# Kernel optimization log

Hardware: AMD Instinct MI355X
Metric: run time of the kernel (lower is better)

The kernel has to match this reference:

```python
import jax, jax.numpy as jnp
import numpy as np

UNITS = 1024
IN_DIM = 1024
BATCH = 8192


def setup_inputs() -> dict:
    key = jax.random.key(0)
    ks = jax.random.split(key, 8)
    return {
        "inputs": jax.random.normal(ks[0], (BATCH, IN_DIM), dtype=jnp.float32),
        "c_prev": jax.random.normal(ks[1], (BATCH, UNITS), dtype=jnp.float32),
        "h_prev": jax.random.normal(ks[2], (BATCH, UNITS), dtype=jnp.float32),
        "kernel": jax.random.normal(ks[3], (IN_DIM, 4 * UNITS), dtype=jnp.float32) * 0.02,
        "recurrent_kernel": jax.random.normal(ks[4], (UNITS, 4 * UNITS), dtype=jnp.float32) * 0.02,
        "bias": jnp.zeros((4 * UNITS,), dtype=jnp.float32),
        "peephole_f": jax.random.normal(ks[5], (UNITS,), dtype=jnp.float32) * 0.1,
        "peephole_i": jax.random.normal(ks[6], (UNITS,), dtype=jnp.float32) * 0.1,
        "peephole_o": jax.random.normal(ks[7], (UNITS,), dtype=jnp.float32) * 0.1,
    }


def reference(inputs, c_prev, h_prev, kernel, recurrent_kernel, bias,
              peephole_f, peephole_i, peephole_o):
    # z: [B, 4U] = x @ W + h_prev @ U + b
    z = inputs @ kernel + h_prev @ recurrent_kernel + bias
    z_f, z_i, z_c, z_o = jnp.split(z, 4, axis=1)
    f = jax.nn.sigmoid(z_f + peephole_f * c_prev)
    i = jax.nn.sigmoid(z_i + peephole_i * c_prev)
    c_tilde = jnp.tanh(z_c)
    c = f * c_prev + i * c_tilde
    o = jax.nn.sigmoid(z_o + peephole_o * c)
    h = o * jnp.tanh(c)
    return h, c
```

## Files before the change

### kernel.cpp

```cpp
#include <hip/hip_runtime.h>

typedef unsigned short u16;
typedef __attribute__((ext_vector_type(8))) short bf16x8;
typedef __attribute__((ext_vector_type(4))) float f32x4;

constexpr int BATCH = 8192;
constexpr int UNITS = 1024;
constexpr int K2    = 2048;
constexpr int N4    = 4096;
constexpr int BK    = 64;
constexpr int BM    = 256;
constexpr int BN    = 256;
constexpr int NKT   = K2 / BK;
constexpr int ASZ   = BM * BK;
constexpr int BSZ   = BN * BK;

__device__ __forceinline__ u16 f2bf(float f) {
  unsigned u = __float_as_uint(f);
  u += 0x7fffu + ((u >> 16) & 1u);
  return (u16)(u >> 16);
}

__device__ __forceinline__ void async_copy16(const void* g, void* l) {
  __builtin_amdgcn_global_load_lds(
      (const __attribute__((address_space(1))) void*)g,
      (__attribute__((address_space(3))) void*)l, 16, 0, 0);
}

__global__ __launch_bounds__(256) void cast_fused_kernel(
    const float* __restrict__ x, const float* __restrict__ h,
    const float* __restrict__ W, const float* __restrict__ U,
    u16* __restrict__ A, u16* __restrict__ B) {
  const int tid = threadIdx.x;
  if (blockIdx.x < 2048) {
    __shared__ float lds[64 * 69];
    const int bid = blockIdx.x;
    const int nb  = bid & 63;
    const int kb  = bid >> 6;
    const int n0  = nb * 64;
    const int k0  = kb * 64;
    const int jn  = n0 >> 10;
    const int q0  = (n0 & 1023) >> 4;
    const float* src = (k0 < UNITS) ? (W + (size_t)k0 * N4)
                                    : (U + (size_t)(k0 - UNITS) * N4);
    {
      const int kk  = tid >> 4;
      const int nn4 = (tid & 15) * 4;
#pragma unroll
      for (int r = 0; r < 4; ++r) {
        const int k = kk + r * 16;
        float4 v = *reinterpret_cast<const float4*>(&src[(size_t)k * N4 + n0 + nn4]);
        lds[k * 69 + nn4 + 0] = v.x;
        lds[k * 69 + nn4 + 1] = v.y;
        lds[k * 69 + nn4 + 2] = v.z;
        lds[k * 69 + nn4 + 3] = v.w;
      }
    }
    __syncthreads();
    {
      const int kk4 = (tid & 15) * 4;
#pragma unroll
      for (int pass = 0; pass < 4; ++pass) {
        const int rr  = (tid >> 4) + pass * 16;
        const int q   = q0 + (rr >> 4);
        const int low = rr & 15;
        const int p   = q * 64 + jn * 16 + low;
        union { ushort4 u4; u16 s[4]; } o;
#pragma unroll
        for (int j = 0; j < 4; ++j) o.s[j] = f2bf(lds[(kk4 + j) * 69 + rr]);
        *reinterpret_cast<ushort4*>(&B[(size_t)p * K2 + k0 + kk4]) = o.u4;
      }
    }
  } else {
    const int t0 = (blockIdx.x - 2048) * 256 + tid;
    const int stride = 4096 * 256;
#pragma unroll
    for (int s = 0; s < 4; ++s) {
      const int g = t0 + s * stride;
      const int idx = g * 4;
      const int b = idx >> 11;
      const int k = idx & 2047;
      const float* src = (k < UNITS) ? (x + (size_t)b * UNITS + k)
                                     : (h + (size_t)b * UNITS + (k - UNITS));
      float4 v = *reinterpret_cast<const float4*>(src);
      union { ushort4 u4; u16 sv[4]; } o;
      o.sv[0] = f2bf(v.x); o.sv[1] = f2bf(v.y);
      o.sv[2] = f2bf(v.z); o.sv[3] = f2bf(v.w);
      *reinterpret_cast<ushort4*>(A + idx) = o.u4;
    }
  }
}

__global__ __launch_bounds__(512, 2) void lstm_gemm_kernel(
    const u16* __restrict__ A, const u16* __restrict__ B,
    const float* __restrict__ bias, const float* __restrict__ c_prev,
    const float* __restrict__ pf, const float* __restrict__ pi,
    const float* __restrict__ po,
    float* __restrict__ out_h, float* __restrict__ out_c) {
  __shared__ u16 lds[2 * ASZ + 2 * BSZ];
  u16* const Asb = lds;
  u16* const Bsb = lds + 2 * ASZ;

  const int tid  = threadIdx.x;
  const int lane = tid & 63;
  const int wave = tid >> 6;
  const int quad = lane >> 4;
  const int c    = lane & 15;

  int lin = blockIdx.y * 16 + blockIdx.x;
  lin = (lin & 7) * 64 + (lin >> 3);
  const int m0 = (lin >> 4) * BM;
  const int n0 = (lin & 15) * BN;

  const int wm = (wave >> 2) * 128;
  const int wn = (wave & 3) * 64;

  const int g8   = ((tid & 7) ^ ((tid >> 3) & 7)) * 8;
  const int rowa = tid >> 3;
  const u16* gA = A + (size_t)(m0 + rowa) * K2 + g8;
  const u16* gB = B + (size_t)(n0 + rowa) * K2 + g8;
  const int ldst = tid * 8;

  const int sl0   = (quad ^ (c & 7)) * 8;
  const int sl1   = ((4 + quad) ^ (c & 7)) * 8;
  const int aoff0 = (wm + c) * 64 + sl0;
  const int aoff1 = (wm + c) * 64 + sl1;
  const int boff0 = (wn + c) * 64 + sl0;
  const int boff1 = (wn + c) * 64 + sl1;

  f32x4 acc[8][4] = {};

#pragma unroll
  for (int i = 0; i < 4; ++i) {
    async_copy16(gA + (size_t)i * 64 * K2, &Asb[i * 4096 + ldst]);
    async_copy16(gB + (size_t)i * 64 * K2, &Bsb[i * 4096 + ldst]);
  }
  asm volatile("s_waitcnt vmcnt(0)" ::: "memory");
  __builtin_amdgcn_s_barrier();
  asm volatile("" ::: "memory");

#pragma unroll 2
  for (int kt = 0; kt < NKT; ++kt) {
    const u16* as = &Asb[(kt & 1) * ASZ];
    const u16* bs = &Bsb[(kt & 1) * BSZ];

    if (kt < NKT - 1) {
      u16* sA = &Asb[((kt + 1) & 1) * ASZ];
      u16* sB = &Bsb[((kt + 1) & 1) * BSZ];
      const size_t ok = (size_t)(kt + 1) * BK;
#pragma unroll
      for (int i = 0; i < 4; ++i) {
        async_copy16(gA + ok + (size_t)i * 64 * K2, sA + i * 4096 + ldst);
        async_copy16(gB + ok + (size_t)i * 64 * K2, sB + i * 4096 + ldst);
      }
    }

    bf16x8 bfr[2][4];
#pragma unroll
    for (int jn = 0; jn < 4; ++jn) {
      bfr[0][jn] = *(const bf16x8*)(bs + boff0 + jn * 1024);
      bfr[1][jn] = *(const bf16x8*)(bs + boff1 + jn * 1024);
    }

    bf16x8 areg[2][2][2];
#pragma unroll
    for (int h = 0; h < 2; ++h)
#pragma unroll
      for (int jm = 0; jm < 2; ++jm)
        areg[0][h][jm] = *(const bf16x8*)(as + (h ? aoff1 : aoff0) + jm * 1024);

#pragma unroll
    for (int ph = 0; ph < 4; ++ph) {
      if (ph < 3) {
#pragma unroll
        for (int h = 0; h < 2; ++h)
#pragma unroll
          for (int jm = 0; jm < 2; ++jm)
            areg[(ph + 1) & 1][h][jm] = *(const bf16x8*)(
                as + (h ? aoff1 : aoff0) + (2 * (ph + 1) + jm) * 1024);
      }
      __builtin_amdgcn_s_setprio(1);
#pragma unroll
      for (int jm = 0; jm < 2; ++jm)
#pragma unroll
        for (int jn = 0; jn < 4; ++jn)
          acc[2 * ph + jm][jn] = __builtin_amdgcn_mfma_f32_16x16x32_bf16(
              areg[ph & 1][0][jm], bfr[0][jn], acc[2 * ph + jm][jn], 0, 0, 0);
#pragma unroll
      for (int jm = 0; jm < 2; ++jm)
#pragma unroll
        for (int jn = 0; jn < 4; ++jn)
          acc[2 * ph + jm][jn] = __builtin_amdgcn_mfma_f32_16x16x32_bf16(
              areg[ph & 1][1][jm], bfr[1][jn], acc[2 * ph + jm][jn], 0, 0, 0);
      __builtin_amdgcn_s_setprio(0);
    }

    if (kt < NKT - 1) {
      asm volatile("s_waitcnt vmcnt(0)" ::: "memory");
      __builtin_amdgcn_s_barrier();
      asm volatile("" ::: "memory");
    }
  }

  const int u = ((n0 + wn) >> 2) + c;
  const float bf_ = bias[u];
  const float bi_ = bias[UNITS + u];
  const float bc_ = bias[2 * UNITS + u];
  const float bo_ = bias[3 * UNITS + u];
  const float pfv = pf[u], piv = pi[u], pov = po[u];
  const int mbase = m0 + wm + quad * 4;
#pragma unroll
  for (int jm = 0; jm < 8; ++jm) {
#pragma unroll
    for (int r = 0; r < 4; ++r) {
      const int b = mbase + jm * 16 + r;
      const float cp = c_prev[(size_t)b * UNITS + u];
      const float zf = acc[jm][0][r] + bf_ + pfv * cp;
      const float zi = acc[jm][1][r] + bi_ + piv * cp;
      const float zc = acc[jm][2][r] + bc_;
      const float zo = acc[jm][3][r] + bo_;
      const float fg = 1.f / (1.f + __expf(-zf));
      const float ig = 1.f / (1.f + __expf(-zi));
      const float ct = 1.f - 2.f / (__expf(2.f * zc) + 1.f);
      const float cn = fg * cp + ig * ct;
      const float og = 1.f / (1.f + __expf(-(zo + pov * cn)));
      const float hn = og * (1.f - 2.f / (__expf(2.f * cn) + 1.f));
      out_h[(size_t)b * UNITS + u] = hn;
      out_c[(size_t)b * UNITS + u] = cn;
    }
  }
}

extern "C" void kernel_launch(void* const* d_in, const int* in_sizes, int n_in,
                              void* d_out, int out_size, void* d_ws, size_t ws_size,
                              hipStream_t stream) {
  const float* x      = (const float*)d_in[0];
  const float* c_prev = (const float*)d_in[1];
  const float* h_prev = (const float*)d_in[2];
  const float* W      = (const float*)d_in[3];
  const float* U      = (const float*)d_in[4];
  const float* bias   = (const float*)d_in[5];
  const float* pf     = (const float*)d_in[6];
  const float* pi     = (const float*)d_in[7];
  const float* po     = (const float*)d_in[8];
  float* out_h = (float*)d_out;
  float* out_c = out_h + (size_t)BATCH * UNITS;

  u16* Abf = (u16*)d_ws;
  u16* Bbf = Abf + (size_t)BATCH * K2;

  cast_fused_kernel<<<6144, 256, 0, stream>>>(x, h_prev, W, U, Abf, Bbf);
  lstm_gemm_kernel<<<dim3(N4 / BN, BATCH / BM), 512, 0, stream>>>(
      Abf, Bbf, bias, c_prev, pf, pi, po, out_h, out_c);
}
```

Baseline: 155.3 us.

## Make GEMM persistent over two N tiles and restructure the MFMA/load interleave

The GEMM grid is cut from 512 to 256 blocks, one per CU. Each block computes two N tiles 2048 columns apart, and the first K-tile of the second tile is prefetched during the last iteration of the first. The inner loop is rewritten so the async global-to-LDS copies are split into two halves placed between MFMA groups, with A fragments loaded in smaller chunks. This is meant to remove the wave-quantization tail and the per-block prologue, and to overlap global loads with MFMA work. In exchange, each tile's epilogue runs serially inside the block, and there are fewer blocks to hide latency.

```diff
diff --git a/kernel.cpp b/kernel.cpp
--- a/kernel.cpp
+++ b/kernel.cpp
@@ -107,18 +107,20 @@
   const int quad = lane >> 4;
   const int c    = lane & 15;
 
-  int lin = blockIdx.y * 16 + blockIdx.x;
-  lin = (lin & 7) * 64 + (lin >> 3);
-  const int m0 = (lin >> 4) * BM;
-  const int n0 = (lin & 15) * BN;
+  const int b    = blockIdx.x;
+  const int orig = (b >> 6) * 128 + (b & 63);
+  const int lin  = (orig & 7) * 64 + (orig >> 3);
+  const int m0   = (lin >> 4) * BM;
+  const int n0a  = (lin & 15) * BN;
 
   const int wm = (wave >> 2) * 128;
   const int wn = (wave & 3) * 64;
 
   const int g8   = ((tid & 7) ^ ((tid >> 3) & 7)) * 8;
   const int rowa = tid >> 3;
-  const u16* gA = A + (size_t)(m0 + rowa) * K2 + g8;
-  const u16* gB = B + (size_t)(n0 + rowa) * K2 + g8;
+  const u16* gA  = A + (size_t)(m0 + rowa) * K2 + g8;
+  const u16* gB0 = B + (size_t)(n0a + rowa) * K2 + g8;
+  const u16* gB1 = gB0 + (size_t)2048 * K2;
   const int ldst = tid * 8;
 
   const int sl0   = (quad ^ (c & 7)) * 8;
@@ -128,105 +130,146 @@
   const int boff0 = (wn + c) * 64 + sl0;
   const int boff1 = (wn + c) * 64 + sl1;
 
-  f32x4 acc[8][4] = {};
+  f32x4 acc[8][4];
 
 #pragma unroll
   for (int i = 0; i < 4; ++i) {
     async_copy16(gA + (size_t)i * 64 * K2, &Asb[i * 4096 + ldst]);
-    async_copy16(gB + (size_t)i * 64 * K2, &Bsb[i * 4096 + ldst]);
+    async_copy16(gB0 + (size_t)i * 64 * K2, &Bsb[i * 4096 + ldst]);
   }
   asm volatile("s_waitcnt vmcnt(0)" ::: "memory");
   __builtin_amdgcn_s_barrier();
-  asm volatile("" ::: "memory");
+
+#pragma unroll 1
+  for (int rep = 0; rep < 2; ++rep) {
+    const u16* gBr = rep ? gB1 : gB0;
+#pragma unroll
+    for (int jm = 0; jm < 8; ++jm)
+#pragma unroll
+      for (int jn = 0; jn < 4; ++jn)
+        acc[jm][jn] = (f32x4){0.f, 0.f, 0.f, 0.f};
 
 #pragma unroll 2
-  for (int kt = 0; kt < NKT; ++kt) {
-    const u16* as = &Asb[(kt & 1) * ASZ];
-    const u16* bs = &Bsb[(kt & 1) * BSZ];
-
-    if (kt < NKT - 1) {
+    for (int kt = 0; kt < NKT; ++kt) {
+      const u16* as = &Asb[(kt & 1) * ASZ];
+      const u16* bs = &Bsb[(kt & 1) * BSZ];
       u16* sA = &Asb[((kt + 1) & 1) * ASZ];
       u16* sB = &Bsb[((kt + 1) & 1) * BSZ];
-      const size_t ok = (size_t)(kt + 1) * BK;
-#pragma unroll
-      for (int i = 0; i < 4; ++i) {
-        async_copy16(gA + ok + (size_t)i * 64 * K2, sA + i * 4096 + ldst);
-        async_copy16(gB + ok + (size_t)i * 64 * K2, sB + i * 4096 + ldst);
-      }
-    }
-
-    bf16x8 bfr[2][4];
-#pragma unroll
-    for (int jn = 0; jn < 4; ++jn) {
-      bfr[0][jn] = *(const bf16x8*)(bs + boff0 + jn * 1024);
-      bfr[1][jn] = *(const bf16x8*)(bs + boff1 + jn * 1024);
-    }
-
-    bf16x8 areg[2][2][2];
-#pragma unroll
-    for (int h = 0; h < 2; ++h)
-#pragma unroll
-      for (int jm = 0; jm < 2; ++jm)
-        areg[0][h][jm] = *(const bf16x8*)(as + (h ? aoff1 : aoff0) + jm * 1024);
-
-#pragma unroll
-    for (int ph = 0; ph < 4; ++ph) {
-      if (ph < 3) {
-#pragma unroll
-        for (int h = 0; h < 2; ++h)
-#pragma unroll
-          for (int jm = 0; jm < 2; ++jm)
-            areg[(ph + 1) & 1][h][jm] = *(const bf16x8*)(
-                as + (h ? aoff1 : aoff0) + (2 * (ph + 1) + jm) * 1024);
-      }
-      __builtin_amdgcn_s_setprio(1);
-#pragma unroll
-      for (int jm = 0; jm < 2; ++jm)
-#pragma unroll
-        for (int jn = 0; jn < 4; ++jn)
-          acc[2 * ph + jm][jn] = __builtin_amdgcn_mfma_f32_16x16x32_bf16(
-              areg[ph & 1][0][jm], bfr[0][jn], acc[2 * ph + jm][jn], 0, 0, 0);
-#pragma unroll
-      for (int jm = 0; jm < 2; ++jm)
-#pragma unroll
-        for (int jn = 0; jn < 4; ++jn)
-          acc[2 * ph + jm][jn] = __builtin_amdgcn_mfma_f32_16x16x32_bf16(
-              areg[ph & 1][1][jm], bfr[1][jn], acc[2 * ph + jm][jn], 0, 0, 0);
-      __builtin_amdgcn_s_setprio(0);
-    }
-
-    if (kt < NKT - 1) {
+      const bool last  = (kt == NKT - 1);
+      const bool stage = !last || (rep == 0);
+      const u16* nA = !last ? gA  + (size_t)(kt + 1) * BK : gA;
+      const u16* nB = !last ? gBr + (size_t)(kt + 1) * BK : gB1;
+
+      bf16x8 bq0[4], aq[4];
+#pragma unroll
+      for (int jn = 0; jn < 4; ++jn)
+        bq0[jn] = *(const bf16x8*)(bs + boff0 + jn * 1024);
+#pragma unroll
+      for (int jm = 0; jm < 4; ++jm)
+        aq[jm] = *(const bf16x8*)(as + aoff0 + jm * 1024);
+
+      if (stage) {
+        async_copy16(nA,                      sA + ldst);
+        async_copy16(nA + (size_t)64 * K2,    sA + 4096 + ldst);
+        async_copy16(nB,                      sB + ldst);
+        async_copy16(nB + (size_t)64 * K2,    sB + 4096 + ldst);
+      }
+      bf16x8 ar[4];
+#pragma unroll
+      for (int jm = 0; jm < 4; ++jm)
+        ar[jm] = *(const bf16x8*)(as + aoff0 + (4 + jm) * 1024);
+      __builtin_amdgcn_s_setprio(1);
+#pragma unroll
+      for (int jm = 0; jm < 4; ++jm)
+#pragma unroll
+        for (int jn = 0; jn < 4; ++jn)
+          acc[jm][jn] = __builtin_amdgcn_mfma_f32_16x16x32_bf16(
+              aq[jm], bq0[jn], acc[jm][jn], 0, 0, 0);
+      __builtin_amdgcn_s_setprio(0);
+
+      if (stage) {
+        async_copy16(nA + (size_t)128 * K2,   sA + 8192 + ldst);
+        async_copy16(nA + (size_t)192 * K2,   sA + 12288 + ldst);
+        async_copy16(nB + (size_t)128 * K2,   sB + 8192 + ldst);
+        async_copy16(nB + (size_t)192 * K2,   sB + 12288 + ldst);
+      }
+      bf16x8 bq1[4], ac2[4];
+#pragma unroll
+      for (int jn = 0; jn < 4; ++jn)
+        bq1[jn] = *(const bf16x8*)(bs + boff1 + jn * 1024);
+#pragma unroll
+      for (int jm = 0; jm < 4; ++jm)
+        ac2[jm] = *(const bf16x8*)(as + aoff1 + jm * 1024);
+      __builtin_amdgcn_s_setprio(1);
+#pragma unroll
+      for (int jm = 0; jm < 4; ++jm)
+#pragma unroll
+        for (int jn = 0; jn < 4; ++jn)
+          acc[4 + jm][jn] = __builtin_amdgcn_mfma_f32_16x16x32_bf16(
+              ar[jm], bq0[jn], acc[4 + jm][jn], 0, 0, 0);
+      __builtin_amdgcn_s_setprio(0);
+
+      bf16x8 ad[4];
+#pragma unroll
+      for (int jm = 0; jm < 4; ++jm)
+        ad[jm] = *(const bf16x8*)(as + aoff1 + (4 + jm) * 1024);
+      __builtin_amdgcn_s_setprio(1);
+#pragma unroll
+      for (int jm = 0; jm < 4; ++jm)
+#pragma unroll
+        for (int jn = 0; jn < 4; ++jn)
+          acc[jm][jn] = __builtin_amdgcn_mfma_f32_16x16x32_bf16(
+              ac2[jm], bq1[jn], acc[jm][jn], 0, 0, 0);
+      __builtin_amdgcn_s_setprio(0);
+
+      __builtin_amdgcn_s_setprio(1);
+#pragma unroll
+      for (int jm = 0; jm < 4; ++jm)
+#pragma unroll
+        for (int jn = 0; jn < 4; ++jn)
+          acc[4 + jm][jn] = __builtin_amdgcn_mfma_f32_16x16x32_bf16(
+              ad[jm], bq1[jn], acc[4 + jm][jn], 0, 0, 0);
+      __builtin_amdgcn_s_setprio(0);
+
+      if (!last) {
+        asm volatile("s_waitcnt vmcnt(0)" ::: "memory");
+        __builtin_amdgcn_s_barrier();
+      }
+    }
+
+    {
+      const int n0 = n0a + rep * 2048;
+      const int u = ((n0 + wn) >> 2) + c;
+      const float bf_ = bias[u];
+      const float bi_ = bias[UNITS + u];
+      const float bc_ = bias[2 * UNITS + u];
+      const float bo_ = bias[3 * UNITS + u];
+      const float pfv = pf[u], piv = pi[u], pov = po[u];
+      const int mbase = m0 + wm + quad * 4;
+#pragma unroll
+      for (int jm = 0; jm < 8; ++jm) {
+#pragma unroll
+        for (int r = 0; r < 4; ++r) {
+          const int bb = mbase + jm * 16 + r;
+          const float cp = c_prev[(size_t)bb * UNITS + u];
+          const float zf = acc[jm][0][r] + bf_ + pfv * cp;
+          const float zi = acc[jm][1][r] + bi_ + piv * cp;
+          const float zc = acc[jm][2][r] + bc_;
+          const float zo = acc[jm][3][r] + bo_;
+          const float fg = 1.f / (1.f + __expf(-zf));
+          const float ig = 1.f / (1.f + __expf(-zi));
+          const float ct = 1.f - 2.f / (__expf(2.f * zc) + 1.f);
+          const float cn = fg * cp + ig * ct;
+          const float og = 1.f / (1.f + __expf(-(zo + pov * cn)));
+          const float hn = og * (1.f - 2.f / (__expf(2.f * cn) + 1.f));
+          out_h[(size_t)bb * UNITS + u] = hn;
+          out_c[(size_t)bb * UNITS + u] = cn;
+        }
+      }
+    }
+    if (rep == 0) {
       asm volatile("s_waitcnt vmcnt(0)" ::: "memory");
       __builtin_amdgcn_s_barrier();
-      asm volatile("" ::: "memory");
-    }
-  }
-
-  const int u = ((n0 + wn) >> 2) + c;
-  const float bf_ = bias[u];
-  const float bi_ = bias[UNITS + u];
-  const float bc_ = bias[2 * UNITS + u];
-  const float bo_ = bias[3 * UNITS + u];
-  const float pfv = pf[u], piv = pi[u], pov = po[u];
-  const int mbase = m0 + wm + quad * 4;
-#pragma unroll
-  for (int jm = 0; jm < 8; ++jm) {
-#pragma unroll
-    for (int r = 0; r < 4; ++r) {
-      const int b = mbase + jm * 16 + r;
-      const float cp = c_prev[(size_t)b * UNITS + u];
-      const float zf = acc[jm][0][r] + bf_ + pfv * cp;
-      const float zi = acc[jm][1][r] + bi_ + piv * cp;
-      const float zc = acc[jm][2][r] + bc_;
-      const float zo = acc[jm][3][r] + bo_;
-      const float fg = 1.f / (1.f + __expf(-zf));
-      const float ig = 1.f / (1.f + __expf(-zi));
-      const float ct = 1.f - 2.f / (__expf(2.f * zc) + 1.f);
-      const float cn = fg * cp + ig * ct;
-      const float og = 1.f / (1.f + __expf(-(zo + pov * cn)));
-      const float hn = og * (1.f - 2.f / (__expf(2.f * cn) + 1.f));
-      out_h[(size_t)b * UNITS + u] = hn;
-      out_c[(size_t)b * UNITS + u] = cn;
     }
   }
 }
@@ -250,6 +293,6 @@
   u16* Bbf = Abf + (size_t)BATCH * K2;
 
   cast_fused_kernel<<<6144, 256, 0, stream>>>(x, h_prev, W, U, Abf, Bbf);
-  lstm_gemm_kernel<<<dim3(N4 / BN, BATCH / BM), 512, 0, stream>>>(
+  lstm_gemm_kernel<<<256, 512, 0, stream>>>(
       Abf, Bbf, bias, c_prev, pf, pi, po, out_h, out_c);
 }
```

Result: slower. 200.2 us (+28.9%).

## Shrink GEMM block tile to 128x128 with 4 blocks per CU

Applied to the files above, without the earlier changes.

Reduces the LSTM GEMM block tile from 256x256 to 128x128, with each of 8 waves computing 32x64 instead of 128x64, and raises the occupancy hint to 4 blocks per CU. It switches to a 1D grid with a new swizzle and simplifies the inner loop to two k-halves without A-fragment double buffering. The intent is more blocks in flight to hide latency, at the cost of less data reuse per block, more global/LDS traffic per FLOP and a lower MFMA-to-load ratio.

```diff
diff --git a/kernel.cpp b/kernel.cpp
--- a/kernel.cpp
+++ b/kernel.cpp
@@ -9,8 +9,8 @@
 constexpr int K2    = 2048;
 constexpr int N4    = 4096;
 constexpr int BK    = 64;
-constexpr int BM    = 256;
-constexpr int BN    = 256;
+constexpr int BM    = 128;
+constexpr int BN    = 128;
 constexpr int NKT   = K2 / BK;
 constexpr int ASZ   = BM * BK;
 constexpr int BSZ   = BN * BK;
@@ -91,7 +91,7 @@
   }
 }
 
-__global__ __launch_bounds__(512, 2) void lstm_gemm_kernel(
+__global__ __launch_bounds__(512, 4) void lstm_gemm_kernel(
     const u16* __restrict__ A, const u16* __restrict__ B,
     const float* __restrict__ bias, const float* __restrict__ c_prev,
     const float* __restrict__ pf, const float* __restrict__ pi,
@@ -107,13 +107,13 @@
   const int quad = lane >> 4;
   const int c    = lane & 15;
 
-  int lin = blockIdx.y * 16 + blockIdx.x;
-  lin = (lin & 7) * 64 + (lin >> 3);
-  const int m0 = (lin >> 4) * BM;
-  const int n0 = (lin & 15) * BN;
-
-  const int wm = (wave >> 2) * 128;
-  const int wn = (wave & 3) * 64;
+  const int lin = blockIdx.x;
+  const int swz = (lin & 7) * 256 + (lin >> 3);
+  const int m0  = (swz >> 5) * BM;
+  const int n0  = (swz & 31) * BN;
+
+  const int wm = (wave >> 1) * 32;
+  const int wn = (wave & 1) * 64;
 
   const int g8   = ((tid & 7) ^ ((tid >> 3) & 7)) * 8;
   const int rowa = tid >> 3;
@@ -128,16 +128,15 @@
   const int boff0 = (wn + c) * 64 + sl0;
   const int boff1 = (wn + c) * 64 + sl1;
 
-  f32x4 acc[8][4] = {};
-
-#pragma unroll
-  for (int i = 0; i < 4; ++i) {
+  f32x4 acc[2][4] = {};
+
+#pragma unroll
+  for (int i = 0; i < 2; ++i) {
     async_copy16(gA + (size_t)i * 64 * K2, &Asb[i * 4096 + ldst]);
     async_copy16(gB + (size_t)i * 64 * K2, &Bsb[i * 4096 + ldst]);
   }
   asm volatile("s_waitcnt vmcnt(0)" ::: "memory");
   __builtin_amdgcn_s_barrier();
-  asm volatile("" ::: "memory");
 
 #pragma unroll 2
   for (int kt = 0; kt < NKT; ++kt) {
@@ -149,56 +148,49 @@
       u16* sB = &Bsb[((kt + 1) & 1) * BSZ];
       const size_t ok = (size_t)(kt + 1) * BK;
 #pragma unroll
-      for (int i = 0; i < 4; ++i) {
+      for (int i = 0; i < 2; ++i) {
         async_copy16(gA + ok + (size_t)i * 64 * K2, sA + i * 4096 + ldst);
         async_copy16(gB + ok + (size_t)i * 64 * K2, sB + i * 4096 + ldst);
       }
     }
 
-    bf16x8 bfr[2][4];
-#pragma unroll
-    for (int jn = 0; jn < 4; ++jn) {
-      bfr[0][jn] = *(const bf16x8*)(bs + boff0 + jn * 1024);
-      bfr[1][jn] = *(const bf16x8*)(bs + boff1 + jn * 1024);
-    }
-
-    bf16x8 areg[2][2][2];
-#pragma unroll
-    for (int h = 0; h < 2; ++h)
-#pragma unroll
-      for (int jm = 0; jm < 2; ++jm)
-        areg[0][h][jm] = *(const bf16x8*)(as + (h ? aoff1 : aoff0) + jm * 1024);
-
-#pragma unroll
-    for (int ph = 0; ph < 4; ++ph) {
-      if (ph < 3) {
-#pragma unroll
-        for (int h = 0; h < 2; ++h)
-#pragma unroll
-          for (int jm = 0; jm < 2; ++jm)
-            areg[(ph + 1) & 1][h][jm] = *(const bf16x8*)(
-                as + (h ? aoff1 : aoff0) + (2 * (ph + 1) + jm) * 1024);
-      }
-      __builtin_amdgcn_s_setprio(1);
-#pragma unroll
-      for (int jm = 0; jm < 2; ++jm)
-#pragma unroll
-        for (int jn = 0; jn < 4; ++jn)
-          acc[2 * ph + jm][jn] = __builtin_amdgcn_mfma_f32_16x16x32_bf16(
-              areg[ph & 1][0][jm], bfr[0][jn], acc[2 * ph + jm][jn], 0, 0, 0);
-#pragma unroll
-      for (int jm = 0; jm < 2; ++jm)
-#pragma unroll
-        for (int jn = 0; jn < 4; ++jn)
-          acc[2 * ph + jm][jn] = __builtin_amdgcn_mfma_f32_16x16x32_bf16(
-              areg[ph & 1][1][jm], bfr[1][jn], acc[2 * ph + jm][jn], 0, 0, 0);
-      __builtin_amdgcn_s_setprio(0);
-    }
+    bf16x8 bq0[4], aq0[2];
+#pragma unroll
+    for (int jn = 0; jn < 4; ++jn)
+      bq0[jn] = *(const bf16x8*)(bs + boff0 + jn * 1024);
+#pragma unroll
+    for (int jm = 0; jm < 2; ++jm)
+      aq0[jm] = *(const bf16x8*)(as + aoff0 + jm * 1024);
+
+    bf16x8 bq1[4], aq1[2];
+#pragma unroll
+    for (int jn = 0; jn < 4; ++jn)
+      bq1[jn] = *(const bf16x8*)(bs + boff1 + jn * 1024);
+#pragma unroll
+    for (int jm = 0; jm < 2; ++jm)
+      aq1[jm] = *(const bf16x8*)(as + aoff1 + jm * 1024);
+
+    __builtin_amdgcn_s_setprio(1);
+#pragma unroll
+    for (int jm = 0; jm < 2; ++jm)
+#pragma unroll
+      for (int jn = 0; jn < 4; ++jn)
+        acc[jm][jn] = __builtin_amdgcn_mfma_f32_16x16x32_bf16(
+            aq0[jm], bq0[jn], acc[jm][jn], 0, 0, 0);
+    __builtin_amdgcn_s_setprio(0);
+
+    __builtin_amdgcn_s_setprio(1);
+#pragma unroll
+    for (int jm = 0; jm < 2; ++jm)
+#pragma unroll
+      for (int jn = 0; jn < 4; ++jn)
+        acc[jm][jn] = __builtin_amdgcn_mfma_f32_16x16x32_bf16(
+            aq1[jm], bq1[jn], acc[jm][jn], 0, 0, 0);
+    __builtin_amdgcn_s_setprio(0);
 
     if (kt < NKT - 1) {
       asm volatile("s_waitcnt vmcnt(0)" ::: "memory");
       __builtin_amdgcn_s_barrier();
-      asm volatile("" ::: "memory");
     }
   }
 
@@ -210,7 +202,7 @@
   const float pfv = pf[u], piv = pi[u], pov = po[u];
   const int mbase = m0 + wm + quad * 4;
 #pragma unroll
-  for (int jm = 0; jm < 8; ++jm) {
+  for (int jm = 0; jm < 2; ++jm) {
 #pragma unroll
     for (int r = 0; r < 4; ++r) {
       const int b = mbase + jm * 16 + r;
@@ -250,6 +242,6 @@
   u16* Bbf = Abf + (size_t)BATCH * K2;
 
   cast_fused_kernel<<<6144, 256, 0, stream>>>(x, h_prev, W, U, Abf, Bbf);
-  lstm_gemm_kernel<<<dim3(N4 / BN, BATCH / BM), 512, 0, stream>>>(
+  lstm_gemm_kernel<<<(BATCH / BM) * (N4 / BN), 512, 0, stream>>>(
       Abf, Bbf, bias, c_prev, pf, pi, po, out_h, out_c);
 }
```

New measurement: 170.5 us. +9.8%, slower.
